# Kernel optimization log

Measured on AMD Instinct MI355X. Metric: run time of the kernel, lower is better.

The kernel has to match this reference:

```python
import jax, jax.numpy as jnp
import numpy as np

N = 50000
DIM = 768   # input_dim == feature dim (self.L)
D_ATT = 128 # self.D


def setup_inputs() -> dict:
    key = jax.random.key(0)
    ks = jax.random.split(key, 6)
    s = lambda fan_in: 1.0 / np.sqrt(fan_in)
    return {
        "x": jax.random.normal(ks[0], (1, N, DIM), dtype=jnp.float32),
        "W_feat": jax.random.normal(ks[1], (DIM, DIM), dtype=jnp.float32) * s(DIM),
        "b_feat": jax.random.normal(ks[2], (DIM,), dtype=jnp.float32) * s(DIM),
        "W_a": jax.random.normal(ks[3], (D_ATT, DIM), dtype=jnp.float32) * s(DIM),
        "W_b": jax.random.normal(ks[4], (D_ATT, DIM), dtype=jnp.float32) * s(DIM),
        "W_c": jax.random.normal(ks[5], (1, D_ATT), dtype=jnp.float32) * s(D_ATT),
    }


def reference(x, W_feat, b_feat, W_a, W_b, W_c):
    # x: [1, N, DIM] -> squeeze bag dim -> [N, DIM]
    h = jax.nn.relu(jnp.einsum('nd,ed->ne', x[0], W_feat) + b_feat)  # [N, 768]
    a = jax.nn.relu(jnp.einsum('nd,kd->nk', h, W_a))      # [N, 128]
    b = jax.nn.sigmoid(jnp.einsum('nd,kd->nk', h, W_b))   # [N, 128]
    logits = jnp.einsum('nk,ok->on', a * b, W_c)           # [1, N] (transpose fused)
    A = jax.nn.softmax(logits, axis=-1)                    # [1, N]
    return jnp.einsum('on,nd->od', A, h)                   # [1, 768]
```

## Files before the change

### kernel.cpp

```cpp
#include <hip/hip_runtime.h>
#include <hip/hip_bf16.h>
#include <stdint.h>

#define DEVINL __device__ __forceinline__

using bf16x8 = __attribute__((ext_vector_type(8))) short;
using f32x4  = __attribute__((ext_vector_type(4))) float;

static constexpr int NPTS = 50000;
static constexpr int NPAD = 50176;
static constexpr int DIM  = 768;
static constexpr int DATT = 128;
static constexpr int NRB  = NPAD / 128;

DEVINL ushort f2b(float f) {
  uint32_t u = __float_as_uint(f);
  u += 0x7fffu + ((u >> 16) & 1u);
  return (ushort)(u >> 16);
}
DEVINL float b2f(ushort u) { return __uint_as_float(((uint32_t)u) << 16); }

DEVINL void gload_lds16(const void* g, void* l) {
  __builtin_amdgcn_global_load_lds((const __attribute__((address_space(1))) void*)g,
                                   (__attribute__((address_space(3))) void*)l,
                                   16, 0, 0);
}

__global__ void cvt8_kernel(const float* __restrict__ src, ushort* __restrict__ dst,
                            int n8_src, int n8_dst) {
  const int stride = gridDim.x * blockDim.x;
  for (int i = blockIdx.x * blockDim.x + threadIdx.x; i < n8_dst; i += stride) {
    float4 v0 = {0.f, 0.f, 0.f, 0.f}, v1 = {0.f, 0.f, 0.f, 0.f};
    if (i < n8_src) {
      const float4* s4 = (const float4*)src;
      v0 = s4[(long)i * 2];
      v1 = s4[(long)i * 2 + 1];
    }
    ushort4 o0 = { f2b(v0.x), f2b(v0.y), f2b(v0.z), f2b(v0.w) };
    ushort4 o1 = { f2b(v1.x), f2b(v1.y), f2b(v1.z), f2b(v1.w) };
    ((ushort4*)dst)[(long)i * 2]     = o0;
    ((ushort4*)dst)[(long)i * 2 + 1] = o1;
  }
}

__global__ void cvt_weights_kernel(const float* __restrict__ Wf, const float* __restrict__ Wa,
                                   const float* __restrict__ Wb,
                                   ushort* __restrict__ wfb, ushort* __restrict__ wab,
                                   ushort* __restrict__ wbb) {
  const int NF = DIM * DIM / 8, NA = DATT * DIM / 8;
  int i = blockIdx.x * blockDim.x + threadIdx.x;
  const float* src; ushort* dst; int j;
  if (i < NF)               { src = Wf; dst = wfb; j = i; }
  else if (i < NF + NA)     { src = Wa; dst = wab; j = i - NF; }
  else if (i < NF + 2 * NA) { src = Wb; dst = wbb; j = i - NF - NA; }
  else return;
  const float4* s4 = (const float4*)src;
  float4 v0 = s4[(long)j * 2];
  float4 v1 = s4[(long)j * 2 + 1];
  ushort4 o0 = { f2b(v0.x), f2b(v0.y), f2b(v0.z), f2b(v0.w) };
  ushort4 o1 = { f2b(v1.x), f2b(v1.y), f2b(v1.z), f2b(v1.w) };
  ((ushort4*)dst)[(long)j * 2]     = o0;
  ((ushort4*)dst)[(long)j * 2 + 1] = o1;
}

__global__ __launch_bounds__(512)
void gemm_h_kernel(const ushort* __restrict__ A, const ushort* __restrict__ B,
                   const float* __restrict__ bias, ushort* __restrict__ H) {
  __shared__ ushort lds[3][24576];

  const int tid  = threadIdx.x;
  const int wid  = tid >> 6;
  const int lane = tid & 63;

  const int bid  = blockIdx.x;
  const int wgid = (bid & 7) * 147 + (bid >> 3);
  const int row0 = (wgid / 6) * 256;
  const int col0 = (wgid % 6) * 128;

  const int wrow = (wid >> 1) * 64;
  const int wcol = (wid & 1) * 64;

  const int srow = lane >> 3;
  const int scol = ((lane & 7) ^ (lane >> 3)) * 8;

  const ushort* Abase = A + (long)row0 * DIM;
  const ushort* Bbase = B + (long)col0 * DIM;

  auto stage = [&](int t, int buf) {
    const int k0 = t * 64;
#pragma unroll
    for (int i = 0; i < 4; ++i) {
      const int ch = i * 8 + wid;
      gload_lds16(Abase + (long)(ch * 8 + srow) * DIM + k0 + scol,
                  &lds[buf][ch * 512]);
    }
#pragma unroll
    for (int i = 0; i < 2; ++i) {
      const int ch = i * 8 + wid;
      gload_lds16(Bbase + (long)(ch * 8 + srow) * DIM + k0 + scol,
                  &lds[buf][16384 + ch * 512]);
    }
  };

  f32x4 acc[4][4] = {};

  stage(0, 0);
  stage(1, 1);
  int c = 0;
  for (int t = 0; t < 12; ++t) {
    if (t < 10) {
      const int nb = (c == 0) ? 2 : c - 1;
      stage(t + 2, nb);
      asm volatile("s_waitcnt vmcnt(12)" ::: "memory");
    } else if (t == 10) {
      asm volatile("s_waitcnt vmcnt(6)" ::: "memory");
    } else {
      asm volatile("s_waitcnt vmcnt(0)" ::: "memory");
    }
    __builtin_amdgcn_s_barrier();
    __builtin_amdgcn_sched_barrier(0);

    const ushort* Ab = &lds[c][0];
    const ushort* Bb = &lds[c][16384];
#pragma unroll
    for (int kk = 0; kk < 2; ++kk) {
      const int j = kk * 4 + (lane >> 4);
      bf16x8 a[4];
#pragma unroll
      for (int m = 0; m < 4; ++m) {
        const int ra = wrow + m * 16 + (lane & 15);
        a[m] = *(const bf16x8*)(Ab + ra * 64 + ((j ^ (ra & 7)) << 3));
      }
#pragma unroll
      for (int n = 0; n < 4; ++n) {
        const int rb = wcol + n * 16 + (lane & 15);
        bf16x8 b = *(const bf16x8*)(Bb + rb * 64 + ((j ^ (rb & 7)) << 3));
#pragma unroll
        for (int m = 0; m < 4; ++m)
          acc[m][n] = __builtin_amdgcn_mfma_f32_16x16x32_bf16(a[m], b, acc[m][n], 0, 0, 0);
      }
    }
    __builtin_amdgcn_sched_barrier(0);
    __builtin_amdgcn_s_barrier();
    c = (c == 2) ? 0 : c + 1;
  }

  const int lq = lane >> 4;
  const int lc = lane & 15;
#pragma unroll
  for (int n = 0; n < 4; ++n) {
    const int cg = col0 + wcol + n * 16 + lc;
    const float bv = bias[cg];
#pragma unroll
    for (int m = 0; m < 4; ++m) {
      const int rg = row0 + wrow + m * 16 + lq * 4;
#pragma unroll
      for (int r2 = 0; r2 < 4; ++r2) {
        float v = acc[m][n][r2] + bv;
        v = fmaxf(v, 0.0f);
        H[(long)(rg + r2) * DIM + cg] = f2b(v);
      }
    }
  }
}

__global__ __launch_bounds__(512)
void gate_kernel(const ushort* __restrict__ Hm, const ushort* __restrict__ Wa,
                 const ushort* __restrict__ Wb, const float* __restrict__ Wc,
                 float* __restrict__ logits) {
  __shared__ ushort Hs [128 * 64];
  __shared__ ushort Was[128 * 64];
  __shared__ ushort Wbs[128 * 64];
  const int tid  = threadIdx.x;
  const int wid  = tid >> 6;
  const int lane = tid & 63;
  const int row0 = blockIdx.x * 128;

  f32x4 fa[8] = {};
  f32x4 fb[8] = {};

  const int ld_r = lane >> 3;
  const int ld_c = (lane & 7) * 8;

  for (int k0 = 0; k0 < DIM; k0 += 64) {
    __syncthreads();
#pragma unroll
    for (int i = 0; i < 2; ++i) {
      const int ch = i * 8 + wid;
      const int r  = ch * 8 + ld_r;
      gload_lds16(Hm + (long)(row0 + r) * DIM + k0 + ld_c, Hs  + ch * 512);
      gload_lds16(Wa + (long)r * DIM        + k0 + ld_c, Was + ch * 512);
      gload_lds16(Wb + (long)r * DIM        + k0 + ld_c, Wbs + ch * 512);
    }
    __syncthreads();
#pragma unroll
    for (int kk = 0; kk < 2; ++kk) {
      const int kc = kk * 32 + (lane >> 4) * 8;
      bf16x8 h = *(const bf16x8*)(Hs + (wid * 16 + (lane & 15)) * 64 + kc);
#pragma unroll
      for (int n = 0; n < 8; ++n) {
        bf16x8 wa = *(const bf16x8*)(Was + (n * 16 + (lane & 15)) * 64 + kc);
        bf16x8 wb = *(const bf16x8*)(Wbs + (n * 16 + (lane & 15)) * 64 + kc);
        fa[n] = __builtin_amdgcn_mfma_f32_16x16x32_bf16(h, wa, fa[n], 0, 0, 0);
        fb[n] = __builtin_amdgcn_mfma_f32_16x16x32_bf16(h, wb, fb[n], 0, 0, 0);
      }
    }
  }

  const int lc = lane & 15;
  const int lq = lane >> 4;
  float g[4];
#pragma unroll
  for (int r = 0; r < 4; ++r) {
    float s = 0.f;
#pragma unroll
    for (int n = 0; n < 8; ++n) {
      float av = fmaxf(fa[n][r], 0.f);
      float sg = 1.f / (1.f + expf(-fb[n][r]));
      s += av * sg * Wc[n * 16 + lc];
    }
    s += __shfl_xor(s, 1);
    s += __shfl_xor(s, 2);
    s += __shfl_xor(s, 4);
    s += __shfl_xor(s, 8);
    g[r] = s;
  }
  if (lc == 0) {
    const int rbase = row0 + wid * 16 + lq * 4;
#pragma unroll
    for (int r = 0; r < 4; ++r) {
      const int nidx = rbase + r;
      if (nidx < NPTS) logits[nidx] = g[r];
    }
  }
}

__global__ __launch_bounds__(1024)
void softmax_stats_kernel(const float* __restrict__ logits, float* __restrict__ stats) {
  __shared__ float red[1024];
  const int tid = threadIdx.x;
  float m = -1e30f;
  for (int i = tid; i < NPTS; i += 1024) m = fmaxf(m, logits[i]);
  red[tid] = m; __syncthreads();
  for (int s = 512; s > 0; s >>= 1) {
    if (tid < s) red[tid] = fmaxf(red[tid], red[tid + s]);
    __syncthreads();
  }
  m = red[0];
  __syncthreads();
  float sum = 0.f;
  for (int i = tid; i < NPTS; i += 1024) sum += expf(logits[i] - m);
  red[tid] = sum; __syncthreads();
  for (int s = 512; s > 0; s >>= 1) {
    if (tid < s) red[tid] += red[tid + s];
    __syncthreads();
  }
  if (tid == 0) { stats[0] = m; stats[1] = red[0]; }
}

__global__ __launch_bounds__(192)
void weighted_partial_kernel(const ushort* __restrict__ Hm, const float* __restrict__ logits,
                             const float* __restrict__ stats, float* __restrict__ part) {
  __shared__ float w[128];
  const int b = blockIdx.x, tid = threadIdx.x;
  const int n0 = b * 128;
  if (tid < 128) {
    const int n = n0 + tid;
    w[tid] = (n < NPTS) ? expf(logits[n] - stats[0]) : 0.f;
  }
  __syncthreads();
  float4 acc = {0.f, 0.f, 0.f, 0.f};
  const ushort* hp = Hm + (long)n0 * DIM + tid * 4;
#pragma unroll 4
  for (int r = 0; r < 128; ++r) {
    const float wr = w[r];
    ushort4 v = *(const ushort4*)(hp + (long)r * DIM);
    acc.x += wr * b2f(v.x);
    acc.y += wr * b2f(v.y);
    acc.z += wr * b2f(v.z);
    acc.w += wr * b2f(v.w);
  }
  ((float4*)(part + (long)b * DIM))[tid] = acc;
}

__global__ void final_reduce_kernel(const float* __restrict__ part,
                                    const float* __restrict__ stats,
                                    float* __restrict__ out) {
  const int c = blockIdx.x * blockDim.x + threadIdx.x;
  if (c >= DIM) return;
  float s = 0.f;
  for (int b = 0; b < NRB; ++b) s += part[(long)b * DIM + c];
  out[c] = s / stats[1];
}

extern "C" void kernel_launch(void* const* d_in, const int* in_sizes, int n_in,
                              void* d_out, int out_size, void* d_ws, size_t ws_size,
                              hipStream_t stream) {
  const float* x  = (const float*)d_in[0];
  const float* Wf = (const float*)d_in[1];
  const float* bf = (const float*)d_in[2];
  const float* Wa = (const float*)d_in[3];
  const float* Wb = (const float*)d_in[4];
  const float* Wc = (const float*)d_in[5];
  float* out = (float*)d_out;

  char* p = (char*)d_ws;
  ushort* xb  = (ushort*)p; p += (size_t)NPAD * DIM * 2;
  ushort* hb  = (ushort*)p; p += (size_t)NPAD * DIM * 2;
  ushort* wfb = (ushort*)p; p += (size_t)DIM * DIM * 2;
  ushort* wab = (ushort*)p; p += (size_t)DATT * DIM * 2;
  ushort* wbb = (ushort*)p; p += (size_t)DATT * DIM * 2;
  float* logits = (float*)p; p += (size_t)NPAD * 4;
  float* stats  = (float*)p; p += 256;
  float* part   = (float*)p; p += (size_t)NRB * DIM * 4;

  cvt8_kernel<<<2048, 256, 0, stream>>>(x, xb, NPTS * DIM / 8, NPAD * DIM / 8);
  cvt_weights_kernel<<<384, 256, 0, stream>>>(Wf, Wa, Wb, wfb, wab, wbb);

  gemm_h_kernel<<<196 * 6, 512, 0, stream>>>(xb, wfb, bf, hb);
  gate_kernel<<<NRB, 512, 0, stream>>>(hb, wab, wbb, Wc, logits);
  softmax_stats_kernel<<<1, 1024, 0, stream>>>(logits, stats);
  weighted_partial_kernel<<<NRB, 192, 0, stream>>>(hb, logits, stats, part);
  final_reduce_kernel<<<3, 256, 0, stream>>>(part, stats, out);
}
```

Measured before the change: 225.7 us.

## Fuse fp32-to-bf16 conversion of x into the feature GEMM mainloop

Drops the separate kernel that converts x to bf16. The GEMM now reads fp32 x straight from global memory into registers, converts it to bf16 and writes it into swizzled LDS, using a register-staged double buffer with two LDS slots instead of the three-slot async global-to-LDS pipeline. This avoids writing and re-reading a roughly 77MB bf16 copy of x, but each tile now reads x in fp32 (the grid has 6 column tiles per row block, so x is read up to six times). It also adds more VGPR pressure and conversion ALU work in the mainloop, and raises MFMA priority with s_setprio.

```diff
diff --git a/kernel.cpp b/kernel.cpp
--- a/kernel.cpp
+++ b/kernel.cpp
@@ -19,28 +19,14 @@
   return (ushort)(u >> 16);
 }
 DEVINL float b2f(ushort u) { return __uint_as_float(((uint32_t)u) << 16); }
+DEVINL uint32_t pk2(float lo, float hi) {
+  return (uint32_t)f2b(lo) | ((uint32_t)f2b(hi) << 16);
+}
 
 DEVINL void gload_lds16(const void* g, void* l) {
   __builtin_amdgcn_global_load_lds((const __attribute__((address_space(1))) void*)g,
                                    (__attribute__((address_space(3))) void*)l,
                                    16, 0, 0);
-}
-
-__global__ void cvt8_kernel(const float* __restrict__ src, ushort* __restrict__ dst,
-                            int n8_src, int n8_dst) {
-  const int stride = gridDim.x * blockDim.x;
-  for (int i = blockIdx.x * blockDim.x + threadIdx.x; i < n8_dst; i += stride) {
-    float4 v0 = {0.f, 0.f, 0.f, 0.f}, v1 = {0.f, 0.f, 0.f, 0.f};
-    if (i < n8_src) {
-      const float4* s4 = (const float4*)src;
-      v0 = s4[(long)i * 2];
-      v1 = s4[(long)i * 2 + 1];
-    }
-    ushort4 o0 = { f2b(v0.x), f2b(v0.y), f2b(v0.z), f2b(v0.w) };
-    ushort4 o1 = { f2b(v1.x), f2b(v1.y), f2b(v1.z), f2b(v1.w) };
-    ((ushort4*)dst)[(long)i * 2]     = o0;
-    ((ushort4*)dst)[(long)i * 2 + 1] = o1;
-  }
 }
 
 __global__ void cvt_weights_kernel(const float* __restrict__ Wf, const float* __restrict__ Wa,
@@ -64,9 +50,9 @@
 }
 
 __global__ __launch_bounds__(512)
-void gemm_h_kernel(const ushort* __restrict__ A, const ushort* __restrict__ B,
-                   const float* __restrict__ bias, ushort* __restrict__ H) {
-  __shared__ ushort lds[3][24576];
+void gemm_h_fused(const float* __restrict__ X, const ushort* __restrict__ Wfb,
+                  const float* __restrict__ bias, ushort* __restrict__ H) {
+  __shared__ ushort lds[2][24576];
 
   const int tid  = threadIdx.x;
   const int wid  = tid >> 6;
@@ -80,48 +66,52 @@
   const int wrow = (wid >> 1) * 64;
   const int wcol = (wid & 1) * 64;
 
-  const int srow = lane >> 3;
-  const int scol = ((lane & 7) ^ (lane >> 3)) * 8;
-
-  const ushort* Abase = A + (long)row0 * DIM;
-  const ushort* Bbase = B + (long)col0 * DIM;
-
-  auto stage = [&](int t, int buf) {
-    const int k0 = t * 64;
+  const int a_r = tid >> 3;
+  const int a_c = tid & 7;
+  const int b_r = tid >> 2;
+  const int b_c = tid & 3;
+
+  const float4 f4z = {0.f, 0.f, 0.f, 0.f};
+
+  float4 aE[4][2], aO[4][2];
+  uint4  bE[2],    bO[2];
+  f32x4  acc[4][4] = {};
+
+  auto LOADA = [&](float4 (&d)[4][2], int T) {
 #pragma unroll
     for (int i = 0; i < 4; ++i) {
-      const int ch = i * 8 + wid;
-      gload_lds16(Abase + (long)(ch * 8 + srow) * DIM + k0 + scol,
-                  &lds[buf][ch * 512]);
-    }
-#pragma unroll
-    for (int i = 0; i < 2; ++i) {
-      const int ch = i * 8 + wid;
-      gload_lds16(Bbase + (long)(ch * 8 + srow) * DIM + k0 + scol,
-                  &lds[buf][16384 + ch * 512]);
-    }
-  };
-
-  f32x4 acc[4][4] = {};
-
-  stage(0, 0);
-  stage(1, 1);
-  int c = 0;
-  for (int t = 0; t < 12; ++t) {
-    if (t < 10) {
-      const int nb = (c == 0) ? 2 : c - 1;
-      stage(t + 2, nb);
-      asm volatile("s_waitcnt vmcnt(12)" ::: "memory");
-    } else if (t == 10) {
-      asm volatile("s_waitcnt vmcnt(6)" ::: "memory");
-    } else {
-      asm volatile("s_waitcnt vmcnt(0)" ::: "memory");
-    }
-    __builtin_amdgcn_s_barrier();
-    __builtin_amdgcn_sched_barrier(0);
-
-    const ushort* Ab = &lds[c][0];
-    const ushort* Bb = &lds[c][16384];
+      const int rg = row0 + i * 64 + a_r;
+      const float* s = X + (long)rg * DIM + T * 64 + a_c * 8;
+      const bool ok = rg < NPTS;
+      d[i][0] = ok ? *(const float4*)s       : f4z;
+      d[i][1] = ok ? *(const float4*)(s + 4) : f4z;
+    }
+  };
+  auto LOADB = [&](uint4 (&d)[2], int T) {
+    const ushort* s = Wfb + (long)(col0 + b_r) * DIM + T * 64 + b_c * 16;
+#pragma unroll
+    for (int j = 0; j < 2; ++j) d[j] = *(const uint4*)(s + j * 8);
+  };
+  auto CVTW = [&](float4 (&a)[4][2], uint4 (&b)[2], int buf) {
+#pragma unroll
+    for (int i = 0; i < 4; ++i) {
+      const int r = i * 64 + a_r;
+      uint4 o;
+      o.x = pk2(a[i][0].x, a[i][0].y);
+      o.y = pk2(a[i][0].z, a[i][0].w);
+      o.z = pk2(a[i][1].x, a[i][1].y);
+      o.w = pk2(a[i][1].z, a[i][1].w);
+      *(uint4*)&lds[buf][r * 64 + ((a_c ^ (r & 7)) << 3)] = o;
+    }
+#pragma unroll
+    for (int j = 0; j < 2; ++j) {
+      const int ch = b_c * 2 + j;
+      *(uint4*)&lds[buf][16384 + b_r * 64 + ((ch ^ (b_r & 7)) << 3)] = b[j];
+    }
+  };
+  auto COMPUTE = [&](int buf) {
+    const ushort* Ab = &lds[buf][0];
+    const ushort* Bb = &lds[buf][16384];
 #pragma unroll
     for (int kk = 0; kk < 2; ++kk) {
       const int j = kk * 4 + (lane >> 4);
@@ -135,15 +125,41 @@
       for (int n = 0; n < 4; ++n) {
         const int rb = wcol + n * 16 + (lane & 15);
         bf16x8 b = *(const bf16x8*)(Bb + rb * 64 + ((j ^ (rb & 7)) << 3));
+        __builtin_amdgcn_s_setprio(1);
 #pragma unroll
         for (int m = 0; m < 4; ++m)
           acc[m][n] = __builtin_amdgcn_mfma_f32_16x16x32_bf16(a[m], b, acc[m][n], 0, 0, 0);
+        __builtin_amdgcn_s_setprio(0);
       }
     }
+  };
+  auto FENCE = [&]() {
+    asm volatile("s_waitcnt lgkmcnt(0)" ::: "memory");
+    __builtin_amdgcn_s_barrier();
     __builtin_amdgcn_sched_barrier(0);
-    __builtin_amdgcn_s_barrier();
-    c = (c == 2) ? 0 : c + 1;
-  }
+  };
+
+  LOADA(aE, 0); LOADB(bE, 0);
+  CVTW(aE, bE, 0);
+  LOADA(aO, 1); LOADB(bO, 1);
+  FENCE();
+
+#pragma unroll 1
+  for (int tt = 0; tt < 5; ++tt) {
+    const int t = tt * 2;
+    LOADA(aE, t + 2); LOADB(bE, t + 2);
+    CVTW(aO, bO, 1);
+    COMPUTE(0);
+    FENCE();
+    LOADA(aO, t + 3); LOADB(bO, t + 3);
+    CVTW(aE, bE, 0);
+    COMPUTE(1);
+    FENCE();
+  }
+  CVTW(aO, bO, 1);
+  COMPUTE(0);
+  FENCE();
+  COMPUTE(1);
 
   const int lq = lane >> 4;
   const int lc = lane & 15;
@@ -305,7 +321,6 @@
   float* out = (float*)d_out;
 
   char* p = (char*)d_ws;
-  ushort* xb  = (ushort*)p; p += (size_t)NPAD * DIM * 2;
   ushort* hb  = (ushort*)p; p += (size_t)NPAD * DIM * 2;
   ushort* wfb = (ushort*)p; p += (size_t)DIM * DIM * 2;
   ushort* wab = (ushort*)p; p += (size_t)DATT * DIM * 2;
@@ -314,10 +329,9 @@
   float* stats  = (float*)p; p += 256;
   float* part   = (float*)p; p += (size_t)NRB * DIM * 4;
 
-  cvt8_kernel<<<2048, 256, 0, stream>>>(x, xb, NPTS * DIM / 8, NPAD * DIM / 8);
   cvt_weights_kernel<<<384, 256, 0, stream>>>(Wf, Wa, Wb, wfb, wab, wbb);
 
-  gemm_h_kernel<<<196 * 6, 512, 0, stream>>>(xb, wfb, bf, hb);
+  gemm_h_fused<<<196 * 6, 512, 0, stream>>>(x, wfb, bf, hb);
   gate_kernel<<<NRB, 512, 0, stream>>>(hb, wab, wbb, Wc, logits);
   softmax_stats_kernel<<<1, 1024, 0, stream>>>(logits, stats);
   weighted_partial_kernel<<<NRB, 192, 0, stream>>>(hb, logits, stats, part);
```

New measurement: 605.8 us. +168.4%, slower.

## Fuse fp32-to-bf16 conversion of x into the feature GEMM's LDS staging

Applied to the files above, without the earlier changes.

Removes the separate pass that converts x to bf16, along with its workspace buffer. The GEMM now loads fp32 x tiles straight into LDS and packs them to bf16 in registers before the MFMA. Tiles change to 128x256 with a double buffer and 2 blocks per CU, and rows past N are clamped to the last valid row. This removes one full write and read of the bf16 copy of x, but doubles the bytes loaded for the A operand and uses a simpler two-stage pipeline that waits on vmcnt(0) every iteration.

```diff
diff --git a/kernel.cpp b/kernel.cpp
--- a/kernel.cpp
+++ b/kernel.cpp
@@ -26,21 +26,18 @@
                                    16, 0, 0);
 }
 
-__global__ void cvt8_kernel(const float* __restrict__ src, ushort* __restrict__ dst,
-                            int n8_src, int n8_dst) {
-  const int stride = gridDim.x * blockDim.x;
-  for (int i = blockIdx.x * blockDim.x + threadIdx.x; i < n8_dst; i += stride) {
-    float4 v0 = {0.f, 0.f, 0.f, 0.f}, v1 = {0.f, 0.f, 0.f, 0.f};
-    if (i < n8_src) {
-      const float4* s4 = (const float4*)src;
-      v0 = s4[(long)i * 2];
-      v1 = s4[(long)i * 2 + 1];
-    }
-    ushort4 o0 = { f2b(v0.x), f2b(v0.y), f2b(v0.z), f2b(v0.w) };
-    ushort4 o1 = { f2b(v1.x), f2b(v1.y), f2b(v1.z), f2b(v1.w) };
-    ((ushort4*)dst)[(long)i * 2]     = o0;
-    ((ushort4*)dst)[(long)i * 2 + 1] = o1;
-  }
+DEVINL uint32_t cvtpk(float lo, float hi) {
+  union { __hip_bfloat162 h2; uint32_t u; } c;
+  c.h2 = __float22bfloat162_rn(float2{lo, hi});
+  return c.u;
+}
+DEVINL bf16x8 pack8(f32x4 lo, f32x4 hi) {
+  union { uint32_t u[4]; bf16x8 v; } r;
+  r.u[0] = cvtpk(lo[0], lo[1]);
+  r.u[1] = cvtpk(lo[2], lo[3]);
+  r.u[2] = cvtpk(hi[0], hi[1]);
+  r.u[3] = cvtpk(hi[2], hi[3]);
+  return r.v;
 }
 
 __global__ void cvt_weights_kernel(const float* __restrict__ Wf, const float* __restrict__ Wa,
@@ -63,10 +60,10 @@
   ((ushort4*)dst)[(long)j * 2 + 1] = o1;
 }
 
-__global__ __launch_bounds__(512)
-void gemm_h_kernel(const ushort* __restrict__ A, const ushort* __restrict__ B,
-                   const float* __restrict__ bias, ushort* __restrict__ H) {
-  __shared__ ushort lds[3][24576];
+__global__ __launch_bounds__(512, 2)
+void gemm_h_fused(const float* __restrict__ X, const ushort* __restrict__ Wfb,
+                  const float* __restrict__ bias, ushort* __restrict__ H) {
+  __shared__ char lds[2][65536];
 
   const int tid  = threadIdx.x;
   const int wid  = tid >> 6;
@@ -74,54 +71,40 @@
 
   const int bid  = blockIdx.x;
   const int wgid = (bid & 7) * 147 + (bid >> 3);
-  const int row0 = (wgid / 6) * 256;
-  const int col0 = (wgid % 6) * 128;
-
-  const int wrow = (wid >> 1) * 64;
-  const int wcol = (wid & 1) * 64;
-
-  const int srow = lane >> 3;
-  const int scol = ((lane & 7) ^ (lane >> 3)) * 8;
-
-  const ushort* Abase = A + (long)row0 * DIM;
-  const ushort* Bbase = B + (long)col0 * DIM;
-
-  auto stage = [&](int t, int buf) {
+  const int row0 = (wgid / 3) * 128;
+  const int col0 = (wgid % 3) * 256;
+
+  const int wrow = (wid >> 2) * 64;
+  const int wcol = (wid & 3) * 64;
+
+  f32x4 acc[4][4] = {};
+
+  const int rA   = wid * 4 + (lane >> 4);
+  const int swzA = ((lane & 15) ^ (rA & 7)) * 4;
+  const int rB   = wid * 8 + (lane >> 3);
+  const int swzB = ((lane & 7) ^ (rB & 7)) * 8;
+
+  auto STAGE = [&](int t, int buf) {
     const int k0 = t * 64;
+    char* base = &lds[buf][0];
 #pragma unroll
     for (int i = 0; i < 4; ++i) {
-      const int ch = i * 8 + wid;
-      gload_lds16(Abase + (long)(ch * 8 + srow) * DIM + k0 + scol,
-                  &lds[buf][ch * 512]);
-    }
-#pragma unroll
-    for (int i = 0; i < 2; ++i) {
-      const int ch = i * 8 + wid;
-      gload_lds16(Bbase + (long)(ch * 8 + srow) * DIM + k0 + scol,
-                  &lds[buf][16384 + ch * 512]);
+      const int r  = i * 32 + rA;
+      const int rg = row0 + r;
+      const int src = rg < NPTS ? rg : NPTS - 1;
+      gload_lds16(X + (long)src * DIM + k0 + swzA, base + (i * 32 + wid * 4) * 256);
+    }
+#pragma unroll
+    for (int i = 0; i < 4; ++i) {
+      const int r = i * 64 + rB;
+      gload_lds16(Wfb + (long)(col0 + r) * DIM + k0 + swzB,
+                  base + 32768 + (i * 64 + wid * 8) * 128);
     }
   };
 
-  f32x4 acc[4][4] = {};
-
-  stage(0, 0);
-  stage(1, 1);
-  int c = 0;
-  for (int t = 0; t < 12; ++t) {
-    if (t < 10) {
-      const int nb = (c == 0) ? 2 : c - 1;
-      stage(t + 2, nb);
-      asm volatile("s_waitcnt vmcnt(12)" ::: "memory");
-    } else if (t == 10) {
-      asm volatile("s_waitcnt vmcnt(6)" ::: "memory");
-    } else {
-      asm volatile("s_waitcnt vmcnt(0)" ::: "memory");
-    }
-    __builtin_amdgcn_s_barrier();
-    __builtin_amdgcn_sched_barrier(0);
-
-    const ushort* Ab = &lds[c][0];
-    const ushort* Bb = &lds[c][16384];
+  auto COMPUTE = [&](int buf) {
+    const float*  Ab = (const float*)&lds[buf][0];
+    const ushort* Bb = (const ushort*)&lds[buf][32768];
 #pragma unroll
     for (int kk = 0; kk < 2; ++kk) {
       const int j = kk * 4 + (lane >> 4);
@@ -129,7 +112,10 @@
 #pragma unroll
       for (int m = 0; m < 4; ++m) {
         const int ra = wrow + m * 16 + (lane & 15);
-        a[m] = *(const bf16x8*)(Ab + ra * 64 + ((j ^ (ra & 7)) << 3));
+        const int s  = ra & 7;
+        f32x4 lo = *(const f32x4*)(Ab + ra * 64 + (((2 * j)     ^ s) << 2));
+        f32x4 hi = *(const f32x4*)(Ab + ra * 64 + (((2 * j + 1) ^ s) << 2));
+        a[m] = pack8(lo, hi);
       }
 #pragma unroll
       for (int n = 0; n < 4; ++n) {
@@ -140,9 +126,21 @@
           acc[m][n] = __builtin_amdgcn_mfma_f32_16x16x32_bf16(a[m], b, acc[m][n], 0, 0, 0);
       }
     }
+  };
+
+  STAGE(0, 0);
+  asm volatile("s_waitcnt vmcnt(0)" ::: "memory");
+  __builtin_amdgcn_s_barrier();
+  __builtin_amdgcn_sched_barrier(0);
+
+#pragma unroll 1
+  for (int t = 0; t < 12; ++t) {
+    if (t < 11) STAGE(t + 1, (t + 1) & 1);
     __builtin_amdgcn_sched_barrier(0);
+    COMPUTE(t & 1);
+    asm volatile("s_waitcnt vmcnt(0)" ::: "memory");
     __builtin_amdgcn_s_barrier();
-    c = (c == 2) ? 0 : c + 1;
+    __builtin_amdgcn_sched_barrier(0);
   }
 
   const int lq = lane >> 4;
@@ -305,7 +303,6 @@
   float* out = (float*)d_out;
 
   char* p = (char*)d_ws;
-  ushort* xb  = (ushort*)p; p += (size_t)NPAD * DIM * 2;
   ushort* hb  = (ushort*)p; p += (size_t)NPAD * DIM * 2;
   ushort* wfb = (ushort*)p; p += (size_t)DIM * DIM * 2;
   ushort* wab = (ushort*)p; p += (size_t)DATT * DIM * 2;
@@ -314,10 +311,9 @@
   float* stats  = (float*)p; p += 256;
   float* part   = (float*)p; p += (size_t)NRB * DIM * 4;
 
-  cvt8_kernel<<<2048, 256, 0, stream>>>(x, xb, NPTS * DIM / 8, NPAD * DIM / 8);
   cvt_weights_kernel<<<384, 256, 0, stream>>>(Wf, Wa, Wb, wfb, wab, wbb);
 
-  gemm_h_kernel<<<196 * 6, 512, 0, stream>>>(xb, wfb, bf, hb);
+  gemm_h_fused<<<392 * 3, 512, 0, stream>>>(x, wfb, bf, hb);
   gate_kernel<<<NRB, 512, 0, stream>>>(hb, wab, wbb, Wc, logits);
   softmax_stats_kernel<<<1, 1024, 0, stream>>>(logits, stats);
   weighted_partial_kernel<<<NRB, 192, 0, stream>>>(hb, logits, stats, part);
```

New measurement: 220.0 us. 1.03x faster.
